# Kernel tuning notes

Hardware: AMD Instinct MI355X
Metric: run time of the kernel (lower is better)

## Reference

```python
import jax, jax.numpy as jnp
import numpy as np

T, N, H, DIN = 128, 256, 512, 255  # inputs last dim = DIN + 1 (trailing action channel)
PACK = H + 5  # packed state: a(1), loc(1), scale(1), v(1), h(H), p(1)


def setup_inputs() -> dict:
    key = jax.random.key(0)
    ks = jax.random.split(key, 12)
    f32 = jnp.float32
    def rn(k, shape, scale):
        return jax.random.normal(k, shape, dtype=f32) * scale
    si, sh = 1.0 / np.sqrt(DIN), 1.0 / np.sqrt(H)
    return {
        "inputs": jax.random.normal(ks[0], (T, N, DIN + 1), dtype=f32),
        "hx": rn(ks[1], (1, N, PACK), 0.1),
        "eps": jax.random.normal(ks[2], (T, N, 1), dtype=f32),
        "Wih": rn(ks[3], (3 * H, DIN), si),
        "Whh": rn(ks[4], (3 * H, H), sh),
        "bih": jnp.zeros((3 * H,), f32),
        "bhh": jnp.zeros((3 * H,), f32),
        "Wa0": rn(ks[5], (H, H), sh), "ba0": jnp.zeros((H,), f32),
        "Wa1": rn(ks[6], (H, H), sh), "ba1": jnp.zeros((H,), f32),
        "Wloc": rn(ks[7], (1, H), sh), "bloc": jnp.zeros((1,), f32),
        "logstd": jnp.zeros((1,), f32),
        "Wc0": rn(ks[8], (H, H), sh), "bc0": jnp.zeros((H,), f32),
        "Wc1": rn(ks[9], (H, H), sh), "bc1": jnp.zeros((H,), f32),
        "Wv": rn(ks[10], (1, H), sh), "bv": jnp.zeros((1,), f32),
    }


def _forward(inputs, hx, eps, Wih, Whh, bih, bhh, Wa0, ba0, Wa1, ba1,
             Wloc, bloc, logstd, Wc0, bc0, Wc1, bc1, Wv, bv):
    inputs = jax.lax.stop_gradient(inputs)  # module calls inputs.detach()
    obs, actions = inputs[..., :DIN], inputs[..., DIN:]
    hx0 = hx[0]                       # [N, PACK] after squeeze_(0)
    h0 = hx0[:, 4:4 + H]              # initial GRU hidden state
    p = hx0[:, H + 4:H + 5]           # [N,1], passed through unchanged

    def step(h, x_t):
        # PyTorch GRU cell math
        gi = x_t @ Wih.T + bih        # [N, 3H]
        gh = h @ Whh.T + bhh          # [N, 3H]
        ir, iz, in_ = jnp.split(gi, 3, axis=-1)
        hr, hz, hn = jnp.split(gh, 3, axis=-1)
        r = jax.nn.sigmoid(ir + hr)
        z = jax.nn.sigmoid(iz + hz)
        n = jnp.tanh(in_ + r * hn)
        h_new = (1.0 - z) * n + z * h
        return h_new, h_new

    _, hs = jax.lax.scan(step, h0, obs)  # [T, N, H]; hn == h for 1-layer unidir GRU

    def mlp2(x, W0, b0, W1, b1):
        return jnp.tanh(jnp.tanh(x @ W0.T + b0) @ W1.T + b1)

    # heads don't feed back into the recurrence -> apply to all timesteps at once
    loc = mlp2(hs, Wa0, ba0, Wa1, ba1) @ Wloc.T + bloc        # [T, N, 1]
    scale = jnp.broadcast_to(jnp.exp(logstd), loc.shape)      # DiagGaussian scale
    v = mlp2(hs, Wc0, bc0, Wc1, bc1) @ Wv.T + bv              # [T, N, 1]

    # sample_new: replace entries of A where actions < 0 with dist.sample()
    sample = jax.lax.stop_gradient(loc + scale * eps)         # .sample() is non-differentiable
    a = jnp.where(actions < 0, sample, actions)

    p_full = jnp.broadcast_to(p, (T, N, 1))
    # pack() order follows RecurrentState fields: a, loc, scale, v, h, p
    return jnp.concatenate([a, loc, scale, v, hs, p_full], axis=-1)  # [T, N, PACK]


def reference(inputs, hx, eps, Wih, Whh, bih, bhh, Wa0, ba0, Wa1, ba1,
              Wloc, bloc, logstd, Wc0, bc0, Wc1, bc1, Wv, bv):
    packed = _forward(inputs, hx, eps, Wih, Whh, bih, bhh, Wa0, ba0, Wa1, ba1,
                      Wloc, bloc, logstd, Wc0, bc0, Wc1, bc1, Wv, bv)
    return (packed, packed[-1:])
```

## Files before the change

### kernel.cpp

```cpp
#include <hip/hip_runtime.h>

typedef unsigned short u16;
typedef unsigned long long u64;
typedef __bf16 bf16x8 __attribute__((ext_vector_type(8)));
typedef float f32x4 __attribute__((ext_vector_type(4)));

#define T_STEPS 128
#define NB 256
#define HDIM 512
#define DIN_ 255
#define PACK_ 517
#define TN 32768

__device__ __forceinline__ float b2f(u16 u) {
    union { unsigned int i; float f; } v; v.i = ((unsigned int)u) << 16; return v.f;
}
__device__ __forceinline__ u16 f2b(float f) {
    union { float f; unsigned int i; } v; v.f = f;
    unsigned int r = v.i + 0x7FFFu + ((v.i >> 16) & 1u);
    return (u16)(r >> 16);
}
__device__ __forceinline__ float sigm(float x) { return 1.f / (1.f + __expf(-x)); }
__device__ __forceinline__ float ftanh(float x) { return 2.f * sigm(2.f * x) - 1.f; }

__device__ __forceinline__ bf16x8 ldx4_bypass(const u16* p) {
    f32x4 t;
    asm volatile("global_load_dwordx4 %0, %1, off sc0 sc1"
                 : "=v"(t) : "v"(p) : "memory");
    union { f32x4 f; bf16x8 b; } u; u.f = t; return u.b;
}
__device__ __forceinline__ void stx4_bypass(u16* p, bf16x8 v) {
    union { bf16x8 b; f32x4 f; } u; u.b = v;
    asm volatile("global_store_dwordx4 %0, %1, off sc0 sc1"
                 :: "v"(p), "v"(u.f) : "memory");
}
#define WAIT_VMCNT(N) asm volatile("s_waitcnt vmcnt(" #N ")" ::: "memory")
#define WAIT_LGKM0    asm volatile("s_waitcnt lgkmcnt(0)" ::: "memory")

template<int DO_TANH, int K, int MT>
__global__ __launch_bounds__(256) void gemm_bt(const u16* __restrict__ A,
                                               const u16* __restrict__ B,
                                               const float* __restrict__ bias,
                                               u16* __restrict__ C, int N) {
    __shared__ u16 lds[64 * K];
    int n0 = blockIdx.x * 64;
    int w = threadIdx.x >> 6, l = threadIdx.x & 63;
    int la = l & 15, lb = l >> 4;
    for (int idx = threadIdx.x; idx < 8 * K; idx += 256) {
        int kq = idx >> 6, row = idx & 63;
        *(bf16x8*)(lds + (size_t)idx * 8) =
            *(const bf16x8*)(B + (size_t)(n0 + row) * K + kq * 8);
    }
    __syncthreads();
    const u16* bq[4];
    #pragma unroll
    for (int c = 0; c < 4; ++c) bq[c] = lds + ((size_t)lb * 64 + 16 * c + la) * 8;

    for (int mt = 0; mt < MT; ++mt) {
        int m0 = (blockIdx.y * MT + mt) * 64;
        int mw = m0 + 16 * w;
        const u16* Ap = A + (size_t)(mw + la) * K + 8 * lb;
        f32x4 acc[4] = {};
        #pragma unroll
        for (int k0 = 0; k0 < K; k0 += 32) {
            bf16x8 a = *(const bf16x8*)(Ap + k0);
            #pragma unroll
            for (int c = 0; c < 4; ++c)
                acc[c] = __builtin_amdgcn_mfma_f32_16x16x32_bf16(
                    a, *(const bf16x8*)(bq[c] + (size_t)k0 * 64), acc[c], 0, 0, 0);
        }
        #pragma unroll
        for (int c = 0; c < 4; ++c) {
            int n = n0 + 16 * c + la;
            float bv = bias[n];
            #pragma unroll
            for (int r = 0; r < 4; ++r) {
                int m = mw + 4 * lb + r;
                float v = acc[c][r] + bv;
                if (DO_TANH) v = ftanh(v);
                C[(size_t)m * N + n] = f2b(v);
            }
        }
    }
}

__global__ __launch_bounds__(256, 1) void gru_persist(
    const u16* __restrict__ h0b, const float* __restrict__ hx,
    const u16* __restrict__ whh_b, const float* __restrict__ bhh,
    const u16* __restrict__ gi_b, float* __restrict__ out,
    u16* __restrict__ hs_b, unsigned int* __restrict__ bar) {
    extern __shared__ u16 lds[];
    const int tid = threadIdx.x;
    const int b = blockIdx.x >> 4, ksl = blockIdx.x & 15;
    const int ks = ksl * 32, m0 = b * 64;
    const int w = tid >> 6, l = tid & 63;
    const int la = l & 15, lb = l >> 4;
    const int mw = m0 + 16 * w;

    for (int idx = tid; idx < 6144; idx += 256) {
        int kq = idx / 96, row = idx - kq * 96;
        int g = row >> 5, rr = row & 31;
        *(bf16x8*)(lds + (size_t)idx * 8) =
            *(const bf16x8*)(whh_b + (size_t)(g * HDIM + ks + rr) * HDIM + kq * 8);
    }
    const u16* bq[6];
    #pragma unroll
    for (int c = 0; c < 6; ++c) {
        int lr = (c >> 1) * 32 + (c & 1) * 16 + la;
        bq[c] = lds + (size_t)(lb * 96 + lr) * 8;
    }
    float bh[3][2];
    #pragma unroll
    for (int g = 0; g < 3; ++g)
        #pragma unroll
        for (int cc = 0; cc < 2; ++cc)
            bh[g][cc] = bhh[g * HDIM + ks + 16 * cc + la];
    float hp[2][4];
    #pragma unroll
    for (int cc = 0; cc < 2; ++cc)
        #pragma unroll
        for (int r = 0; r < 4; ++r)
            hp[cc][r] = hx[(size_t)(mw + 4 * lb + r) * PACK_ + 4 + ks + 16 * cc + la];

    u16* packbuf = lds + 49152 + w * 512;

    __syncthreads();
    unsigned int* mybar = bar + b * 64;

    for (int t = 0; t < T_STEPS; ++t) {
        const u16* gi_t = gi_b + (size_t)t * NB * 3 * HDIM;

        u16 giv[3][2][4];
        #pragma unroll
        for (int r = 0; r < 4; ++r) {
            const u16* gp = gi_t + (size_t)(mw + 4 * lb + r) * 1536 + ks + la;
            #pragma unroll
            for (int g = 0; g < 3; ++g)
                #pragma unroll
                for (int cc = 0; cc < 2; ++cc)
                    giv[g][cc][r] = gp[g * HDIM + 16 * cc];
        }

        if (t > 0) {
            unsigned tgt = 64u * (unsigned)t;
            while (__hip_atomic_load(mybar, __ATOMIC_RELAXED,
                                     __HIP_MEMORY_SCOPE_AGENT) < tgt)
                __builtin_amdgcn_s_sleep(1);
        }

        const u16* Ap = (t ? hs_b + (size_t)(t - 1) * NB * HDIM : h0b)
                        + (size_t)(mw + la) * HDIM + 8 * lb;
        bf16x8 a[16];
        #pragma unroll
        for (int kk = 0; kk < 16; ++kk) a[kk] = ldx4_bypass(Ap + 32 * kk);

        f32x4 acc[6] = {};
        WAIT_VMCNT(8);
        __builtin_amdgcn_sched_barrier(0);
        #pragma unroll
        for (int kk = 0; kk < 8; ++kk) {
            #pragma unroll
            for (int c = 0; c < 6; ++c)
                acc[c] = __builtin_amdgcn_mfma_f32_16x16x32_bf16(
                    a[kk], *(const bf16x8*)(bq[c] + (size_t)kk * 3072), acc[c], 0, 0, 0);
        }
        WAIT_VMCNT(0);
        __builtin_amdgcn_sched_barrier(0);
        #pragma unroll
        for (int kk = 8; kk < 16; ++kk) {
            #pragma unroll
            for (int c = 0; c < 6; ++c)
                acc[c] = __builtin_amdgcn_mfma_f32_16x16x32_bf16(
                    a[kk], *(const bf16x8*)(bq[c] + (size_t)kk * 3072), acc[c], 0, 0, 0);
        }

        float hnewv[2][4];
        #pragma unroll
        for (int cc = 0; cc < 2; ++cc) {
            #pragma unroll
            for (int r = 0; r < 4; ++r) {
                float hr = acc[0 + cc][r] + bh[0][cc];
                float hz = acc[2 + cc][r] + bh[1][cc];
                float hn = acc[4 + cc][r] + bh[2][cc];
                float rr = sigm(b2f(giv[0][cc][r]) + hr);
                float zz = sigm(b2f(giv[1][cc][r]) + hz);
                float nn = ftanh(b2f(giv[2][cc][r]) + rr * hn);
                float hnew = (1.f - zz) * nn + zz * hp[cc][r];
                hp[cc][r] = hnew;
                hnewv[cc][r] = hnew;
            }
        }

        #pragma unroll
        for (int cc = 0; cc < 2; ++cc) {
            #pragma unroll
            for (int r = 0; r < 4; ++r) {
                float nbv = __shfl_xor(hnewv[cc][r], 1, 64);
                if (!(la & 1)) {
                    unsigned pk = (unsigned)f2b(hnewv[cc][r]) |
                                  ((unsigned)f2b(nbv) << 16);
                    *(unsigned*)(packbuf + (4 * lb + r) * 32 + 16 * cc + la) = pk;
                }
            }
        }
        WAIT_LGKM0;
        __builtin_amdgcn_sched_barrier(0);
        bf16x8 hv = *(const bf16x8*)(packbuf + (l >> 2) * 32 + 8 * (l & 3));
        u16* hs_t = hs_b + (size_t)t * NB * HDIM;
        stx4_bypass(hs_t + (size_t)(m0 + 16 * w + (l >> 2)) * HDIM + ks + 8 * (l & 3), hv);

        WAIT_VMCNT(0);
        if (t < T_STEPS - 1 && l == 0)
            __hip_atomic_fetch_add(mybar, 1u, __ATOMIC_RELAXED,
                                   __HIP_MEMORY_SCOPE_AGENT);

        float* out_t = out + (size_t)t * NB * PACK_;
        #pragma unroll
        for (int cc = 0; cc < 2; ++cc)
            #pragma unroll
            for (int r = 0; r < 4; ++r)
                out_t[(size_t)(mw + 4 * lb + r) * PACK_ + 4 + ks + 16 * cc + la] =
                    hnewv[cc][r];
    }
}

__global__ __launch_bounds__(256) void head_dot(const u16* __restrict__ X,
                                                const u16* __restrict__ W,
                                                const float* __restrict__ b,
                                                float* __restrict__ out, int off) {
    int wid = (int)((blockIdx.x * blockDim.x + threadIdx.x) >> 6);
    int l = threadIdx.x & 63;
    if (wid >= TN) return;
    bf16x8 xv = *(const bf16x8*)(X + (size_t)wid * HDIM + 8 * l);
    bf16x8 wv = *(const bf16x8*)(W + 8 * l);
    float s = 0.f;
    #pragma unroll
    for (int j = 0; j < 8; ++j) s += (float)xv[j] * (float)wv[j];
    #pragma unroll
    for (int d = 32; d; d >>= 1) s += __shfl_down(s, d, 64);
    if (l == 0) out[(size_t)wid * PACK_ + off] = s + b[0];
}

__global__ void prep_w(const float* __restrict__ Wih, const float* __restrict__ Whh,
                       const float* __restrict__ Wa0, const float* __restrict__ Wa1,
                       const float* __restrict__ Wloc, const float* __restrict__ Wc0,
                       const float* __restrict__ Wc1, const float* __restrict__ Wv,
                       const float* __restrict__ hx,
                       u16* Wih_b, u16* Whh_b, u16* Wa0_b, u16* Wa1_b,
                       u16* Wloc_b, u16* Wc0_b, u16* Wc1_b, u16* Wv_b,
                       float* h0f, u16* h0b) {
    int i = blockIdx.x * 256 + threadIdx.x;
    if (i < 1536 * 256) { int r = i >> 8, c = i & 255;
        Wih_b[i] = (c < DIN_) ? f2b(Wih[r * DIN_ + c]) : (u16)0; return; }
    i -= 1536 * 256;
    if (i < 1536 * 512) { Whh_b[i] = f2b(Whh[i]); return; } i -= 1536 * 512;
    if (i < 512 * 512) { Wa0_b[i] = f2b(Wa0[i]); return; } i -= 512 * 512;
    if (i < 512 * 512) { Wa1_b[i] = f2b(Wa1[i]); return; } i -= 512 * 512;
    if (i < 512 * 512) { Wc0_b[i] = f2b(Wc0[i]); return; } i -= 512 * 512;
    if (i < 512 * 512) { Wc1_b[i] = f2b(Wc1[i]); return; } i -= 512 * 512;
    if (i < 512) { Wloc_b[i] = f2b(Wloc[i]); return; } i -= 512;
    if (i < 512) { Wv_b[i] = f2b(Wv[i]); return; } i -= 512;
    if (i < NB * HDIM) { int n = i >> 9, k = i & 511;
        float v = hx[n * PACK_ + 4 + k]; h0f[i] = v; h0b[i] = f2b(v); return; }
}

__global__ void prep_obs(const float* __restrict__ in, u16* __restrict__ obs) {
    int idx = blockIdx.x * 256 + threadIdx.x;
    if (idx >= TN * 32) return;
    int m = idx >> 5, j = idx & 31;
    const float* src = in + (size_t)m * 256 + 8 * j;
    union { u16 s[8]; uint4 u; } t;
    #pragma unroll
    for (int q = 0; q < 8; ++q) t.s[q] = f2b(src[q]);
    if (j == 31) t.s[7] = 0;
    *(uint4*)(obs + (size_t)m * 256 + 8 * j) = t.u;
}

__global__ void finalize_out(const float* __restrict__ in, const float* __restrict__ eps,
                             const float* __restrict__ hx, const float* __restrict__ logstd,
                             float* __restrict__ out) {
    int m = blockIdx.x * 256 + threadIdx.x;
    if (m >= TN) return;
    int n = m & (NB - 1);
    float scale = __expf(logstd[0]);
    float loc = out[(size_t)m * PACK_ + 1];
    float act = in[(size_t)m * 256 + DIN_];
    float a = (act < 0.f) ? (loc + scale * eps[m]) : act;
    out[(size_t)m * PACK_ + 0] = a;
    out[(size_t)m * PACK_ + 2] = scale;
    out[(size_t)m * PACK_ + PACK_ - 1] = hx[n * PACK_ + PACK_ - 1];
}

__global__ void tail_copy(float* __restrict__ out) {
    int i = blockIdx.x * 256 + threadIdx.x;
    if (i >= NB * PACK_) return;
    out[(size_t)T_STEPS * NB * PACK_ + i] = out[(size_t)(T_STEPS - 1) * NB * PACK_ + i];
}

extern "C" void kernel_launch(void* const* d_in, const int* in_sizes, int n_in,
                              void* d_out, int out_size, void* d_ws, size_t ws_size,
                              hipStream_t stream) {
    const float* inputs = (const float*)d_in[0];
    const float* hx     = (const float*)d_in[1];
    const float* eps    = (const float*)d_in[2];
    const float* Wih    = (const float*)d_in[3];
    const float* Whh    = (const float*)d_in[4];
    const float* bih    = (const float*)d_in[5];
    const float* bhh    = (const float*)d_in[6];
    const float* Wa0    = (const float*)d_in[7];
    const float* ba0    = (const float*)d_in[8];
    const float* Wa1    = (const float*)d_in[9];
    const float* ba1    = (const float*)d_in[10];
    const float* Wloc   = (const float*)d_in[11];
    const float* bloc   = (const float*)d_in[12];
    const float* logstd = (const float*)d_in[13];
    const float* Wc0    = (const float*)d_in[14];
    const float* bc0    = (const float*)d_in[15];
    const float* Wc1    = (const float*)d_in[16];
    const float* bc1    = (const float*)d_in[17];
    const float* Wv     = (const float*)d_in[18];
    const float* bv     = (const float*)d_in[19];
    float* out = (float*)d_out;
    char* ws = (char*)d_ws;

    const size_t o_gi   = 0;
    const size_t o_buf0 = 0;
    const size_t o_buf1 = 33554432;
    const size_t o_hs   = 100663296;
    const size_t o_obs  = o_hs + 33554432;
    const size_t o_whh  = o_obs + 16777216;
    const size_t o_wih  = o_whh + 1572864;
    const size_t o_wa0  = o_wih + 786432;
    const size_t o_wa1  = o_wa0 + 524288;
    const size_t o_wc0  = o_wa1 + 524288;
    const size_t o_wc1  = o_wc0 + 524288;
    const size_t o_wloc = o_wc1 + 524288;
    const size_t o_wv   = o_wloc + 1024;
    const size_t o_h0f  = o_wv + 1024;
    const size_t o_h0b  = o_h0f + 524288;
    const size_t o_bar  = o_h0b + 262144;
    const size_t NEED   = o_bar + 4096;
    if (ws_size < NEED) return;

    u16*   gi_b   = (u16*)(ws + o_gi);
    u16*   buf0   = (u16*)(ws + o_buf0);
    u16*   buf1   = (u16*)(ws + o_buf1);
    u16*   hs_b   = (u16*)(ws + o_hs);
    u16*   obs_b  = (u16*)(ws + o_obs);
    u16*   whh_b  = (u16*)(ws + o_whh);
    u16*   wih_b  = (u16*)(ws + o_wih);
    u16*   wa0_b  = (u16*)(ws + o_wa0);
    u16*   wa1_b  = (u16*)(ws + o_wa1);
    u16*   wc0_b  = (u16*)(ws + o_wc0);
    u16*   wc1_b  = (u16*)(ws + o_wc1);
    u16*   wloc_b = (u16*)(ws + o_wloc);
    u16*   wv_b   = (u16*)(ws + o_wv);
    float* h0f    = (float*)(ws + o_h0f);
    u16*   h0b    = (u16*)(ws + o_h0b);
    unsigned int* bar = (unsigned int*)(ws + o_bar);

    static bool attr_set = false;
    if (!attr_set) {
        hipFuncSetAttribute((const void*)gru_persist,
                            hipFuncAttributeMaxDynamicSharedMemorySize, 102400);
        attr_set = true;
    }

    hipMemsetAsync(bar, 0, 4096, stream);

    prep_w<<<9220, 256, 0, stream>>>(Wih, Whh, Wa0, Wa1, Wloc, Wc0, Wc1, Wv, hx,
                                     wih_b, whh_b, wa0_b, wa1_b, wloc_b, wc0_b, wc1_b, wv_b,
                                     h0f, h0b);
    prep_obs<<<4096, 256, 0, stream>>>(inputs, obs_b);

    gemm_bt<0, 256, 8><<<dim3(24, 64), 256, 0, stream>>>(obs_b, wih_b, bih, gi_b, 1536);

    gru_persist<<<64, 256, 102400, stream>>>(h0b, hx, whh_b, bhh, gi_b, out, hs_b, bar);

    gemm_bt<1, 512, 8><<<dim3(8, 64), 256, 0, stream>>>(hs_b, wa0_b, ba0, buf0, 512);
    gemm_bt<1, 512, 8><<<dim3(8, 64), 256, 0, stream>>>(buf0, wa1_b, ba1, buf1, 512);
    head_dot<<<8192, 256, 0, stream>>>(buf1, wloc_b, bloc, out, 1);
    gemm_bt<1, 512, 8><<<dim3(8, 64), 256, 0, stream>>>(hs_b, wc0_b, bc0, buf0, 512);
    gemm_bt<1, 512, 8><<<dim3(8, 64), 256, 0, stream>>>(buf0, wc1_b, bc1, buf1, 512);
    head_dot<<<8192, 256, 0, stream>>>(buf1, wv_b, bv, out, 3);

    finalize_out<<<128, 256, 0, stream>>>(inputs, eps, hx, logstd, out);
    tail_copy<<<518, 256, 0, stream>>>(out);
}
```

Baseline: 1.452 ms.

## Split GRU persistent kernel across 128 blocks with XCC-aware local barriers

The persistent GRU kernel goes from 64 to 128 blocks, each covering 32 batch rows instead of 64. Each block now needs only 16 arrivals per step on its group barrier. Blocks read their XCC id and check whether every block in their batch group sits on the same XCC. If so, they use cache-coherent (non-bypass) loads, stores and atomics for the hidden-state exchange, which avoids cross-die cache bypass latency. The cost is a startup handshake, a block-wide __syncthreads per step, and reliance on co-residency and XCC placement, with a spin guard as a fallback.

```diff
diff --git a/kernel.cpp b/kernel.cpp
--- a/kernel.cpp
+++ b/kernel.cpp
@@ -23,16 +23,10 @@
 __device__ __forceinline__ float sigm(float x) { return 1.f / (1.f + __expf(-x)); }
 __device__ __forceinline__ float ftanh(float x) { return 2.f * sigm(2.f * x) - 1.f; }
 
-__device__ __forceinline__ bf16x8 ldx4_bypass(const u16* p) {
+__device__ __forceinline__ bf16x8 ldx4(const u16* p) {
     f32x4 t;
-    asm volatile("global_load_dwordx4 %0, %1, off sc0 sc1"
-                 : "=v"(t) : "v"(p) : "memory");
+    asm volatile("global_load_dwordx4 %0, %1, off" : "=v"(t) : "v"(p) : "memory");
     union { f32x4 f; bf16x8 b; } u; u.f = t; return u.b;
-}
-__device__ __forceinline__ void stx4_bypass(u16* p, bf16x8 v) {
-    union { bf16x8 b; f32x4 f; } u; u.b = v;
-    asm volatile("global_store_dwordx4 %0, %1, off sc0 sc1"
-                 :: "v"(p), "v"(u.f) : "memory");
 }
 #define WAIT_VMCNT(N) asm volatile("s_waitcnt vmcnt(" #N ")" ::: "memory")
 #define WAIT_LGKM0    asm volatile("s_waitcnt lgkmcnt(0)" ::: "memory")
@@ -90,77 +84,114 @@
     const u16* __restrict__ gi_b, float* __restrict__ out,
     u16* __restrict__ hs_b, unsigned int* __restrict__ bar) {
     extern __shared__ u16 lds[];
+    __shared__ unsigned s_loc;
     const int tid = threadIdx.x;
-    const int b = blockIdx.x >> 4, ksl = blockIdx.x & 15;
-    const int ks = ksl * 32, m0 = b * 64;
+    const int bid = blockIdx.x;
+    const int g = bid & 7, s = bid >> 3;
+    const int ks = s * 32, m0 = g * 32;
     const int w = tid >> 6, l = tid & 63;
     const int la = l & 15, lb = l >> 4;
-    const int mw = m0 + 16 * w;
+    const int rw = w >> 1, cw = w & 1;
+    const int mw = m0 + 16 * rw;
+    const int kc = ks + 16 * cw;
+
+    unsigned myx;
+    asm volatile("s_getreg_b32 %0, hwreg(HW_REG_XCC_ID)" : "=s"(myx));
+    myx = (myx & 15u) + 1u;
+    unsigned int* tbl = bar + 512;
+    if (tid == 0)
+        __hip_atomic_fetch_add(tbl + bid, myx, __ATOMIC_RELAXED,
+                               __HIP_MEMORY_SCOPE_AGENT);
 
     for (int idx = tid; idx < 6144; idx += 256) {
         int kq = idx / 96, row = idx - kq * 96;
-        int g = row >> 5, rr = row & 31;
+        int gg = row >> 5, rr = row & 31;
         *(bf16x8*)(lds + (size_t)idx * 8) =
-            *(const bf16x8*)(whh_b + (size_t)(g * HDIM + ks + rr) * HDIM + kq * 8);
-    }
-    const u16* bq[6];
-    #pragma unroll
-    for (int c = 0; c < 6; ++c) {
-        int lr = (c >> 1) * 32 + (c & 1) * 16 + la;
-        bq[c] = lds + (size_t)(lb * 96 + lr) * 8;
-    }
-    float bh[3][2];
-    #pragma unroll
-    for (int g = 0; g < 3; ++g)
-        #pragma unroll
-        for (int cc = 0; cc < 2; ++cc)
-            bh[g][cc] = bhh[g * HDIM + ks + 16 * cc + la];
-    float hp[2][4];
-    #pragma unroll
-    for (int cc = 0; cc < 2; ++cc)
-        #pragma unroll
-        for (int r = 0; r < 4; ++r)
-            hp[cc][r] = hx[(size_t)(mw + 4 * lb + r) * PACK_ + 4 + ks + 16 * cc + la];
-
-    u16* packbuf = lds + 49152 + w * 512;
-
+            *(const bf16x8*)(whh_b + (size_t)(gg * HDIM + ks + rr) * HDIM + kq * 8);
+    }
+    const u16* bq[3];
+    #pragma unroll
+    for (int c = 0; c < 3; ++c)
+        bq[c] = lds + (size_t)(lb * 96 + c * 32 + 16 * cw + la) * 8;
+    float bh[3];
+    #pragma unroll
+    for (int gg = 0; gg < 3; ++gg) bh[gg] = bhh[gg * HDIM + kc + la];
+    float hp[4];
+    #pragma unroll
+    for (int r = 0; r < 4; ++r)
+        hp[r] = hx[(size_t)(mw + 4 * lb + r) * PACK_ + 4 + kc + la];
+
+    if (tid == 0) {
+        unsigned vals[16];
+        int guard = 0;
+        bool ok;
+        do {
+            ok = true;
+            #pragma unroll
+            for (int k = 0; k < 16; ++k) {
+                vals[k] = __hip_atomic_fetch_add(tbl + g + 8 * k, 0u,
+                                                 __ATOMIC_RELAXED,
+                                                 __HIP_MEMORY_SCOPE_AGENT);
+                ok = ok && (vals[k] != 0u);
+            }
+            if (!ok) __builtin_amdgcn_s_sleep(8);
+        } while (!ok && ++guard < (1 << 16));
+        unsigned lv = ok ? 1u : 0u;
+        #pragma unroll
+        for (int k = 1; k < 16; ++k) lv &= (unsigned)(vals[k] == vals[0]);
+        s_loc = lv;
+    }
+    u16* packbuf = lds + 49152 + w * 256;
     __syncthreads();
-    unsigned int* mybar = bar + b * 64;
+    const bool loc = (s_loc != 0);
+    unsigned int* mybar = bar + g * 64;
 
     for (int t = 0; t < T_STEPS; ++t) {
         const u16* gi_t = gi_b + (size_t)t * NB * 3 * HDIM;
 
-        u16 giv[3][2][4];
+        u16 giv[3][4];
         #pragma unroll
         for (int r = 0; r < 4; ++r) {
-            const u16* gp = gi_t + (size_t)(mw + 4 * lb + r) * 1536 + ks + la;
-            #pragma unroll
-            for (int g = 0; g < 3; ++g)
-                #pragma unroll
-                for (int cc = 0; cc < 2; ++cc)
-                    giv[g][cc][r] = gp[g * HDIM + 16 * cc];
+            const u16* gp = gi_t + (size_t)(mw + 4 * lb + r) * 1536 + kc + la;
+            #pragma unroll
+            for (int gg = 0; gg < 3; ++gg) giv[gg][r] = gp[gg * HDIM];
         }
 
         if (t > 0) {
-            unsigned tgt = 64u * (unsigned)t;
-            while (__hip_atomic_load(mybar, __ATOMIC_RELAXED,
-                                     __HIP_MEMORY_SCOPE_AGENT) < tgt)
+            unsigned tgt = 16u * (unsigned)t;
+            int guard = 0;
+            for (;;) {
+                unsigned v = 0;
+                if (l == 0) {
+                    if (loc)
+                        asm volatile(
+                            "global_atomic_add %0, %1, %2, off sc0\n\t"
+                            "s_waitcnt vmcnt(0)"
+                            : "=v"(v) : "v"(mybar), "v"(0u) : "memory");
+                    else
+                        v = __hip_atomic_fetch_add(mybar, 0u, __ATOMIC_RELAXED,
+                                                   __HIP_MEMORY_SCOPE_AGENT);
+                }
+                v = (unsigned)__builtin_amdgcn_readfirstlane((int)v);
+                if (v >= tgt || ++guard > (1 << 20)) break;
                 __builtin_amdgcn_s_sleep(1);
+            }
+            asm volatile("" ::: "memory");
         }
 
         const u16* Ap = (t ? hs_b + (size_t)(t - 1) * NB * HDIM : h0b)
                         + (size_t)(mw + la) * HDIM + 8 * lb;
         bf16x8 a[16];
         #pragma unroll
-        for (int kk = 0; kk < 16; ++kk) a[kk] = ldx4_bypass(Ap + 32 * kk);
-
-        f32x4 acc[6] = {};
+        for (int kk = 0; kk < 16; ++kk) a[kk] = ldx4(Ap + 32 * kk);
+
+        f32x4 acc[3] = {};
         WAIT_VMCNT(8);
         __builtin_amdgcn_sched_barrier(0);
         #pragma unroll
         for (int kk = 0; kk < 8; ++kk) {
             #pragma unroll
-            for (int c = 0; c < 6; ++c)
+            for (int c = 0; c < 3; ++c)
                 acc[c] = __builtin_amdgcn_mfma_f32_16x16x32_bf16(
                     a[kk], *(const bf16x8*)(bq[c] + (size_t)kk * 3072), acc[c], 0, 0, 0);
         }
@@ -169,58 +200,57 @@
         #pragma unroll
         for (int kk = 8; kk < 16; ++kk) {
             #pragma unroll
-            for (int c = 0; c < 6; ++c)
+            for (int c = 0; c < 3; ++c)
                 acc[c] = __builtin_amdgcn_mfma_f32_16x16x32_bf16(
                     a[kk], *(const bf16x8*)(bq[c] + (size_t)kk * 3072), acc[c], 0, 0, 0);
         }
 
-        float hnewv[2][4];
-        #pragma unroll
-        for (int cc = 0; cc < 2; ++cc) {
-            #pragma unroll
-            for (int r = 0; r < 4; ++r) {
-                float hr = acc[0 + cc][r] + bh[0][cc];
-                float hz = acc[2 + cc][r] + bh[1][cc];
-                float hn = acc[4 + cc][r] + bh[2][cc];
-                float rr = sigm(b2f(giv[0][cc][r]) + hr);
-                float zz = sigm(b2f(giv[1][cc][r]) + hz);
-                float nn = ftanh(b2f(giv[2][cc][r]) + rr * hn);
-                float hnew = (1.f - zz) * nn + zz * hp[cc][r];
-                hp[cc][r] = hnew;
-                hnewv[cc][r] = hnew;
-            }
-        }
-
-        #pragma unroll
-        for (int cc = 0; cc < 2; ++cc) {
-            #pragma unroll
-            for (int r = 0; r < 4; ++r) {
-                float nbv = __shfl_xor(hnewv[cc][r], 1, 64);
-                if (!(la & 1)) {
-                    unsigned pk = (unsigned)f2b(hnewv[cc][r]) |
-                                  ((unsigned)f2b(nbv) << 16);
-                    *(unsigned*)(packbuf + (4 * lb + r) * 32 + 16 * cc + la) = pk;
-                }
+        float hnewv[4];
+        #pragma unroll
+        for (int r = 0; r < 4; ++r) {
+            float rr2 = sigm(b2f(giv[0][r]) + acc[0][r] + bh[0]);
+            float zz  = sigm(b2f(giv[1][r]) + acc[1][r] + bh[1]);
+            float nn  = ftanh(b2f(giv[2][r]) + rr2 * (acc[2][r] + bh[2]));
+            float hnew = (1.f - zz) * nn + zz * hp[r];
+            hp[r] = hnew;
+            hnewv[r] = hnew;
+        }
+
+        #pragma unroll
+        for (int r = 0; r < 4; ++r) {
+            float nbv = __shfl_xor(hnewv[r], 1, 64);
+            if (!(la & 1)) {
+                unsigned pk = (unsigned)f2b(hnewv[r]) | ((unsigned)f2b(nbv) << 16);
+                *(unsigned*)(packbuf + (4 * lb + r) * 16 + la) = pk;
             }
         }
         WAIT_LGKM0;
         __builtin_amdgcn_sched_barrier(0);
-        bf16x8 hv = *(const bf16x8*)(packbuf + (l >> 2) * 32 + 8 * (l & 3));
         u16* hs_t = hs_b + (size_t)t * NB * HDIM;
-        stx4_bypass(hs_t + (size_t)(m0 + 16 * w + (l >> 2)) * HDIM + ks + 8 * (l & 3), hv);
-
+        if (l < 32) {
+            bf16x8 hv = *(const bf16x8*)(packbuf + (l >> 1) * 16 + 8 * (l & 1));
+            union { bf16x8 b; f32x4 f; } u; u.b = hv;
+            u16* sp = hs_t + (size_t)(mw + (l >> 1)) * HDIM + kc + 8 * (l & 1);
+            if (loc) asm volatile("global_store_dwordx4 %0, %1, off"
+                                  :: "v"(sp), "v"(u.f) : "memory");
+            else     asm volatile("global_store_dwordx4 %0, %1, off sc0 sc1"
+                                  :: "v"(sp), "v"(u.f) : "memory");
+        }
         WAIT_VMCNT(0);
-        if (t < T_STEPS - 1 && l == 0)
-            __hip_atomic_fetch_add(mybar, 1u, __ATOMIC_RELAXED,
-                                   __HIP_MEMORY_SCOPE_AGENT);
+        __syncthreads();
+        if (t < T_STEPS - 1 && tid == 0) {
+            if (loc)
+                asm volatile("global_atomic_add %0, %1, off"
+                             :: "v"(mybar), "v"(1u) : "memory");
+            else
+                __hip_atomic_fetch_add(mybar, 1u, __ATOMIC_RELAXED,
+                                       __HIP_MEMORY_SCOPE_AGENT);
+        }
 
         float* out_t = out + (size_t)t * NB * PACK_;
         #pragma unroll
-        for (int cc = 0; cc < 2; ++cc)
-            #pragma unroll
-            for (int r = 0; r < 4; ++r)
-                out_t[(size_t)(mw + 4 * lb + r) * PACK_ + 4 + ks + 16 * cc + la] =
-                    hnewv[cc][r];
+        for (int r = 0; r < 4; ++r)
+            out_t[(size_t)(mw + 4 * lb + r) * PACK_ + 4 + kc + la] = hnewv[r];
     }
 }
 
@@ -375,7 +405,7 @@
 
     gemm_bt<0, 256, 8><<<dim3(24, 64), 256, 0, stream>>>(obs_b, wih_b, bih, gi_b, 1536);
 
-    gru_persist<<<64, 256, 102400, stream>>>(h0b, hx, whh_b, bhh, gi_b, out, hs_b, bar);
+    gru_persist<<<128, 256, 102400, stream>>>(h0b, hx, whh_b, bhh, gi_b, out, hs_b, bar);
 
     gemm_bt<1, 512, 8><<<dim3(8, 64), 256, 0, stream>>>(hs_b, wa0_b, ba0, buf0, 512);
     gemm_bt<1, 512, 8><<<dim3(8, 64), 256, 0, stream>>>(buf0, wa1_b, ba1, buf1, 512);
```

Measured after the change: 1.515 ms. 1.04x slower.
